# Optimization experiments

Measured on AMD Instinct MI355X. Metric: run time of the kernel, lower is better.

Reference implementation:

```python
import jax, jax.numpy as jnp
import numpy as np

B, T, C = 32, 1024, 1024
MAX_LEN = 2 * T  # static upper bound: durations < 3 per token is not assumed; durations in {0,1,2} => sum <= 2T


def setup_inputs() -> dict:
    key = jax.random.key(0)
    k1, k2, k3 = jax.random.split(key, 3)
    x = jax.random.normal(k1, (B, T, C), dtype=jnp.float32)
    durations = jax.random.randint(k2, (B, T), 0, 3, dtype=jnp.int32)
    seq_lengths = jax.random.randint(k3, (B,), T // 2, T + 1, dtype=jnp.int32)
    return {"x": x, "durations": durations, "seq_lengths": seq_lengths, "max_len": MAX_LEN}


def reference(x, durations, seq_lengths, max_len):
    # Mask durations beyond each sequence's valid length (torch: durations * mask.float())
    Bt, Tt, _ = x.shape
    tok_mask = jnp.arange(Tt)[None, :] < seq_lengths[:, None]           # [B, T]
    d = jnp.where(tok_mask, durations, 0).astype(jnp.int32)             # [B, T]

    # Cumulative end-offset of each token's expanded span; cum[b, t] = end position of token t
    cum = jnp.cumsum(d, axis=1)                                         # [B, T]
    total = cum[:, -1]                                                  # [B] valid output frames

    # For each output frame p, the source token is the first t with cum[t] > p.
    # side='right' correctly skips zero-duration tokens.
    pos = jnp.arange(max_len)                                           # [max_len]
    t_idx = jax.vmap(lambda c: jnp.searchsorted(c, pos, side='right'))(cum)  # [B, max_len]
    t_idx = jnp.minimum(t_idx, Tt - 1)

    out = jnp.take_along_axis(x, t_idx[:, :, None], axis=1)             # [B, max_len, C]
    valid = (pos[None, :] < total[:, None])[:, :, None]                 # zero-pad past total frames
    return jnp.where(valid, out, jnp.zeros((), x.dtype))
```

## Files before the change

### kernel.cpp

```cpp
#include <hip/hip_runtime.h>

#define BB 32
#define TT 1024
#define CC 1024
#define ML 2048

__global__ __launch_bounds__(TT) void lr_scan_scatter(const int* __restrict__ dur,
                                                      const int* __restrict__ seqlen,
                                                      int* __restrict__ tidx) {
    __shared__ int buf[2][TT];
    const int b = blockIdx.x;
    const int t = threadIdx.x;
    const int sl = seqlen[b];
    const int d = (t < sl) ? dur[b * TT + t] : 0;
    buf[0][t] = d;
    __syncthreads();
    int src = 0;
    for (int off = 1; off < TT; off <<= 1) {
        int v = buf[src][t];
        if (t >= off) v += buf[src][t - off];
        buf[src ^ 1][t] = v;
        __syncthreads();
        src ^= 1;
    }
    const int end   = buf[src][t];
    const int start = end - d;
    int* __restrict__ row = tidx + b * ML;
    for (int p = start; p < end; ++p)
        row[p] = t;
    const int total = buf[src][TT - 1];
    for (int p = total + t; p < ML; p += TT)
        row[p] = -1;
}

__global__ __launch_bounds__(256) void lr_gather(const float* __restrict__ x,
                                                 const int* __restrict__ tidx,
                                                 float4* __restrict__ out) {
    const int row = blockIdx.x;
    const int b   = row >> 11;
    const int t   = tidx[row];
    float4 v = make_float4(0.f, 0.f, 0.f, 0.f);
    if (t >= 0) {
        const float4* __restrict__ xrow =
            (const float4*)(x + ((size_t)b * TT + t) * CC);
        v = xrow[threadIdx.x];
    }
    out[(size_t)row * (CC / 4) + threadIdx.x] = v;
}

extern "C" void kernel_launch(void* const* d_in, const int* in_sizes, int n_in,
                              void* d_out, int out_size, void* d_ws, size_t ws_size,
                              hipStream_t stream) {
    const float* x   = (const float*)d_in[0];
    const int*   dur = (const int*)d_in[1];
    const int*   sl  = (const int*)d_in[2];
    float* out  = (float*)d_out;
    int*   tidx = (int*)d_ws;

    lr_scan_scatter<<<BB, TT, 0, stream>>>(dur, sl, tidx);
    lr_gather<<<BB * ML, 256, 0, stream>>>(x, tidx, (float4*)out);
}
```

Baseline: 63.69 us.

## Use wave-shuffle scan and gather four rows per block with nontemporal stores

The scan kernel now runs 256 threads, each handling four durations, and uses wavefront shuffles plus a small shared-memory combine. This replaces the 10-step shared-memory Hillis-Steele scan and its repeated barriers. The gather kernel handles four output rows per block, reading their indices with one int4 load, and writes the output with nontemporal stores. This is meant to cut block scheduling overhead and avoid polluting the cache with the 256MB output stream. The scatter loops are now serialized per thread over four tokens, and the per-block work grows.

```diff
diff --git a/kernel.cpp b/kernel.cpp
--- a/kernel.cpp
+++ b/kernel.cpp
@@ -5,47 +5,77 @@
 #define CC 1024
 #define ML 2048
 
-__global__ __launch_bounds__(TT) void lr_scan_scatter(const int* __restrict__ dur,
-                                                      const int* __restrict__ seqlen,
-                                                      int* __restrict__ tidx) {
-    __shared__ int buf[2][TT];
-    const int b = blockIdx.x;
-    const int t = threadIdx.x;
-    const int sl = seqlen[b];
-    const int d = (t < sl) ? dur[b * TT + t] : 0;
-    buf[0][t] = d;
+typedef float vfloat4 __attribute__((ext_vector_type(4)));
+
+__global__ __launch_bounds__(256) void lr_scan_scatter(const int* __restrict__ dur,
+                                                       const int* __restrict__ seqlen,
+                                                       int* __restrict__ tidx) {
+    const int b    = blockIdx.x;
+    const int tid  = threadIdx.x;
+    const int lane = tid & 63;
+    const int wave = tid >> 6;
+    const int sl   = seqlen[b];
+    const int base = tid * 4;
+
+    const int4 dv = ((const int4*)(dur + b * TT))[tid];
+    const int d0 = (base + 0 < sl) ? dv.x : 0;
+    const int d1 = (base + 1 < sl) ? dv.y : 0;
+    const int d2 = (base + 2 < sl) ? dv.z : 0;
+    const int d3 = (base + 3 < sl) ? dv.w : 0;
+    const int local = d0 + d1 + d2 + d3;
+
+    int v = local;
+    #pragma unroll
+    for (int off = 1; off < 64; off <<= 1) {
+        const int n = __shfl_up(v, off, 64);
+        if (lane >= off) v += n;
+    }
+
+    __shared__ int wsum[4];
+    __shared__ int s_total;
+    if (lane == 63) wsum[wave] = v;
     __syncthreads();
-    int src = 0;
-    for (int off = 1; off < TT; off <<= 1) {
-        int v = buf[src][t];
-        if (t >= off) v += buf[src][t - off];
-        buf[src ^ 1][t] = v;
-        __syncthreads();
-        src ^= 1;
-    }
-    const int end   = buf[src][t];
-    const int start = end - d;
+    int woff = 0;
+    #pragma unroll
+    for (int w = 0; w < 3; ++w)
+        if (w < wave) woff += wsum[w];
+
+    const int excl = woff + v - local;
+    const int c0 = excl + d0;
+    const int c1 = c0 + d1;
+    const int c2 = c1 + d2;
+    const int c3 = c2 + d3;
+
     int* __restrict__ row = tidx + b * ML;
-    for (int p = start; p < end; ++p)
-        row[p] = t;
-    const int total = buf[src][TT - 1];
-    for (int p = total + t; p < ML; p += TT)
-        row[p] = -1;
+    for (int p = excl; p < c0; ++p) row[p] = base + 0;
+    for (int p = c0;   p < c1; ++p) row[p] = base + 1;
+    for (int p = c1;   p < c2; ++p) row[p] = base + 2;
+    for (int p = c2;   p < c3; ++p) row[p] = base + 3;
+
+    if (tid == 255) s_total = c3;
+    __syncthreads();
+    const int total = s_total;
+    for (int p = total + tid; p < ML; p += 256) row[p] = -1;
 }
 
 __global__ __launch_bounds__(256) void lr_gather(const float* __restrict__ x,
                                                  const int* __restrict__ tidx,
-                                                 float4* __restrict__ out) {
-    const int row = blockIdx.x;
-    const int b   = row >> 11;
-    const int t   = tidx[row];
-    float4 v = make_float4(0.f, 0.f, 0.f, 0.f);
-    if (t >= 0) {
-        const float4* __restrict__ xrow =
-            (const float4*)(x + ((size_t)b * TT + t) * CC);
-        v = xrow[threadIdx.x];
+                                                 vfloat4* __restrict__ out) {
+    const int r0 = blockIdx.x * 4;
+    const int b  = r0 >> 11;
+    const int4 tv = ((const int4*)tidx)[blockIdx.x];
+    const int ts[4] = {tv.x, tv.y, tv.z, tv.w};
+
+    const vfloat4* __restrict__ xb = (const vfloat4*)(x + (size_t)b * TT * CC);
+    vfloat4* __restrict__ o = out + (size_t)r0 * (CC / 4) + threadIdx.x;
+
+    #pragma unroll
+    for (int i = 0; i < 4; ++i) {
+        const int t = ts[i];
+        vfloat4 v = (vfloat4)(0.f);
+        if (t >= 0) v = xb[(size_t)t * (CC / 4) + threadIdx.x];
+        __builtin_nontemporal_store(v, o + i * (CC / 4));
     }
-    out[(size_t)row * (CC / 4) + threadIdx.x] = v;
 }
 
 extern "C" void kernel_launch(void* const* d_in, const int* in_sizes, int n_in,
@@ -57,6 +87,6 @@
     float* out  = (float*)d_out;
     int*   tidx = (int*)d_ws;
 
-    lr_scan_scatter<<<BB, TT, 0, stream>>>(dur, sl, tidx);
-    lr_gather<<<BB * ML, 256, 0, stream>>>(x, tidx, (float4*)out);
+    lr_scan_scatter<<<BB, 256, 0, stream>>>(dur, sl, tidx);
+    lr_gather<<<(BB * ML) / 4, 256, 0, stream>>>(x, tidx, (vfloat4*)out);
 }
```

Result: faster. 54.23 us (-14.9%).
